# Kernel tuning notes

Measured on AMD Instinct MI355X. Metric: run time of the kernel, lower is better.

## Reference

```python
import jax, jax.numpy as jnp
import numpy as np

DIM = 384
RED = 16
PAIR = 128
EPS = 1e-5


def setup_inputs() -> dict:
    key = jax.random.key(0)
    ks = jax.random.split(key, 6)
    b, m = 2, 512
    x = jax.random.normal(ks[0], (b, m, DIM), dtype=jnp.float32)
    ln_gamma = jnp.ones((DIM,), dtype=jnp.float32)
    ln_beta = jnp.zeros((DIM,), dtype=jnp.float32)
    w_red = jax.random.normal(ks[1], (DIM, RED), dtype=jnp.float32) / np.sqrt(DIM)
    b_red = jax.random.normal(ks[2], (RED,), dtype=jnp.float32) * 0.02
    w_out = jax.random.normal(ks[3], (RED * RED, PAIR), dtype=jnp.float32) / np.sqrt(RED * RED)
    b_out = jax.random.normal(ks[4], (PAIR,), dtype=jnp.float32) * 0.02
    return {"x": x, "ln_gamma": ln_gamma, "ln_beta": ln_beta,
            "w_red": w_red, "b_red": b_red, "w_out": w_out, "b_out": b_out}


def reference(x, ln_gamma, ln_beta, w_red, b_red, w_out, b_out):
    # LayerNorm over last dim (eps=1e-5, torch default)
    mu = jnp.mean(x, axis=-1, keepdims=True)
    var = jnp.mean(jnp.square(x - mu), axis=-1, keepdims=True)
    xn = (x - mu) * jax.lax.rsqrt(var + EPS) * ln_gamma + ln_beta
    # Linear dim -> 16
    xr = jnp.einsum('bmd,dr->bmr', xn, w_red) + b_red  # (b, m, 16)
    # Full pairwise outer product + projection: same math as
    # einsum('bmi,bnj->bmnij') -> reshape (i j) -> Linear(256, pair_dim),
    # fused so the (i,j) axes contract directly with w_out reshaped to (16,16,pair).
    wr = w_out.reshape(RED, RED, PAIR)
    out = jnp.einsum('bmi,bnj,ijp->bmnp', xr, xr, wr) + b_out  # (b, m, m, pair)
    return out
```

## Files before the change

kernel.cpp:

```cpp
#include <hip/hip_runtime.h>
#include <hip/hip_bf16.h>

#define DIM 384
#define RED 16
#define PAIR 128
#define B 2
#define M 512
#define EPSV 1e-5f

typedef float f32x4 __attribute__((ext_vector_type(4)));
typedef short bf16x8 __attribute__((ext_vector_type(8)));

__device__ __forceinline__ unsigned short f2bf(float f) {
  union { float f; unsigned u; } v; v.f = f;
  unsigned r = v.u + 0x7fffu + ((v.u >> 16) & 1u);
  return (unsigned short)(r >> 16);
}

__global__ __launch_bounds__(128) void opm_k1(
    const float* __restrict__ x, const float* __restrict__ g,
    const float* __restrict__ be, const float* __restrict__ w_red,
    const float* __restrict__ b_red, const float* __restrict__ w_out,
    unsigned short* __restrict__ xr_bf, unsigned short* __restrict__ T_bf) {
  const int row = blockIdx.x;
  const int tid = threadIdx.x;
  const float* xrow = x + (size_t)row * DIM;

  __shared__ float xn[DIM];
  __shared__ float xr_s[RED];
  __shared__ float rs[2][2];
  __shared__ float psum[8][RED];

  float v0 = xrow[tid];
  float v1 = xrow[tid + 128];
  float v2 = xrow[tid + 256];
  float s  = v0 + v1 + v2;
  float sq = v0 * v0 + v1 * v1 + v2 * v2;
  #pragma unroll
  for (int off = 32; off > 0; off >>= 1) {
    s  += __shfl_down(s, off);
    sq += __shfl_down(sq, off);
  }
  if ((tid & 63) == 0) { rs[0][tid >> 6] = s; rs[1][tid >> 6] = sq; }
  __syncthreads();
  const float mean = (rs[0][0] + rs[0][1]) * (1.0f / DIM);
  const float var  = (rs[1][0] + rs[1][1]) * (1.0f / DIM) - mean * mean;
  const float rstd = rsqrtf(var + EPSV);

  xn[tid]       = (v0 - mean) * rstd * g[tid]       + be[tid];
  xn[tid + 128] = (v1 - mean) * rstd * g[tid + 128] + be[tid + 128];
  xn[tid + 256] = (v2 - mean) * rstd * g[tid + 256] + be[tid + 256];
  __syncthreads();

  {
    const int r = tid & 15;
    const int part = tid >> 4;
    float ps = 0.0f;
    const int d0 = part * 48;
    #pragma unroll 8
    for (int d = d0; d < d0 + 48; ++d) ps += xn[d] * w_red[d * RED + r];
    psum[part][r] = ps;
  }
  __syncthreads();
  if (tid < RED) {
    float v = b_red[tid];
    #pragma unroll
    for (int q = 0; q < 8; ++q) v += psum[q][tid];
    xr_s[tid] = v;
    xr_bf[(size_t)row * RED + tid] = f2bf(v);
  }
  __syncthreads();

  {
    const int p = tid;
    const float* W = w_out + p;
    float acc[RED];
    #pragma unroll
    for (int i = 0; i < RED; ++i) {
      float a = 0.0f;
      #pragma unroll
      for (int j = 0; j < RED; ++j) a += xr_s[j] * W[(i * RED + j) * PAIR];
      acc[i] = a;
    }
    unsigned int w0[4], w1[4];
    #pragma unroll
    for (int k = 0; k < 4; ++k) {
      w0[k] = (unsigned)f2bf(acc[2*k])     | ((unsigned)f2bf(acc[2*k+1]) << 16);
      w1[k] = (unsigned)f2bf(acc[8+2*k])   | ((unsigned)f2bf(acc[8+2*k+1]) << 16);
    }
    unsigned int* dst = (unsigned int*)(T_bf + ((size_t)row * PAIR + p) * RED);
    #pragma unroll
    for (int k = 0; k < 4; ++k) { dst[k] = w0[k]; dst[4+k] = w1[k]; }
  }
}

__global__ __launch_bounds__(256) void opm_k2(
    const unsigned short* __restrict__ xr_bf, const unsigned short* __restrict__ T_bf,
    const float* __restrict__ b_out, float* __restrict__ out) {
  const int nb = blockIdx.x & 127;
  const int mt = (blockIdx.x >> 7) & 7;
  const int b  = blockIdx.x >> 10;
  const int wave = threadIdx.x >> 6;
  const int lane = threadIdx.x & 63;
  const int q = lane >> 4;
  const int r = lane & 15;
  const int n = nb * 4 + wave;

  bf16x8 bv[8];
  const unsigned short* Tb = T_bf + ((size_t)(b * M + n) * PAIR) * RED;
  #pragma unroll
  for (int pb = 0; pb < 8; ++pb) {
    bf16x8 v = {0, 0, 0, 0, 0, 0, 0, 0};
    if (q < 2) v = *(const bf16x8*)(Tb + (pb * 16 + r) * RED + q * 8);
    bv[pb] = v;
  }
  float bias[8];
  #pragma unroll
  for (int pb = 0; pb < 8; ++pb) bias[pb] = b_out[pb * 16 + r];

  const size_t MROW = (size_t)M * PAIR;

  #pragma unroll
  for (int ms = 0; ms < 4; ++ms) {
    const int m0 = mt * 64 + ms * 16;
    bf16x8 av = {0, 0, 0, 0, 0, 0, 0, 0};
    if (q < 2) av = *(const bf16x8*)(xr_bf + (size_t)(b * M + m0 + r) * RED + q * 8);

    float* outbase = out + ((size_t)(b * M + m0 + q * 4) * M + n) * PAIR + r;
    #pragma unroll
    for (int pb = 0; pb < 8; ++pb) {
      f32x4 acc = {bias[pb], bias[pb], bias[pb], bias[pb]};
      acc = __builtin_amdgcn_mfma_f32_16x16x32_bf16(av, bv[pb], acc, 0, 0, 0);
      float* o = outbase + pb * 16;
      o[0]        = acc[0];
      o[MROW]     = acc[1];
      o[2 * MROW] = acc[2];
      o[3 * MROW] = acc[3];
    }
  }
}

extern "C" void kernel_launch(void* const* d_in, const int* in_sizes, int n_in,
                              void* d_out, int out_size, void* d_ws, size_t ws_size,
                              hipStream_t stream) {
  const float* x       = (const float*)d_in[0];
  const float* ln_g    = (const float*)d_in[1];
  const float* ln_b    = (const float*)d_in[2];
  const float* w_red   = (const float*)d_in[3];
  const float* b_red   = (const float*)d_in[4];
  const float* w_out   = (const float*)d_in[5];
  const float* b_out   = (const float*)d_in[6];
  float* out = (float*)d_out;

  unsigned short* xr_bf = (unsigned short*)d_ws;
  unsigned short* T_bf  = xr_bf + (size_t)B * M * RED;

  opm_k1<<<B * M, 128, 0, stream>>>(x, ln_g, ln_b, w_red, b_red, w_out, xr_bf, T_bf);
  opm_k2<<<B * (M / 64) * (M / 4), 256, 0, stream>>>(xr_bf, T_bf, b_out, out);
}
```

Measured before the change: 57.32 us.

## Stage MFMA output through LDS for vectorized stores; two rows per k1 block

```diff
diff --git a/kernel.cpp b/kernel.cpp
--- a/kernel.cpp
+++ b/kernel.cpp
@@ -7,6 +7,7 @@
 #define B 2
 #define M 512
 #define EPSV 1e-5f
+#define LSTR 133
 
 typedef float f32x4 __attribute__((ext_vector_type(4)));
 typedef short bf16x8 __attribute__((ext_vector_type(8)));
@@ -22,75 +23,81 @@
     const float* __restrict__ be, const float* __restrict__ w_red,
     const float* __restrict__ b_red, const float* __restrict__ w_out,
     unsigned short* __restrict__ xr_bf, unsigned short* __restrict__ T_bf) {
-  const int row = blockIdx.x;
-  const int tid = threadIdx.x;
-  const float* xrow = x + (size_t)row * DIM;
+  const int row0 = blockIdx.x * 2;
+  const int tid  = threadIdx.x;
+  const int wave = tid >> 6;
+  const int lane = tid & 63;
 
-  __shared__ float xn[DIM];
-  __shared__ float xr_s[RED];
-  __shared__ float rs[2][2];
-  __shared__ float psum[8][RED];
+  __shared__ float xn_s[2][DIM];
+  __shared__ float xr_s[2][RED];
+  __shared__ float psum[2][4][RED];
 
-  float v0 = xrow[tid];
-  float v1 = xrow[tid + 128];
-  float v2 = xrow[tid + 256];
-  float s  = v0 + v1 + v2;
-  float sq = v0 * v0 + v1 * v1 + v2 * v2;
-  #pragma unroll
-  for (int off = 32; off > 0; off >>= 1) {
-    s  += __shfl_down(s, off);
-    sq += __shfl_down(sq, off);
+  {
+    const int row = row0 + wave;
+    const float* xrow = x + (size_t)row * DIM;
+    float v[6];
+    #pragma unroll
+    for (int k = 0; k < 6; ++k) v[k] = xrow[lane + 64 * k];
+    float s = 0.f, sq = 0.f;
+    #pragma unroll
+    for (int k = 0; k < 6; ++k) { s += v[k]; sq += v[k] * v[k]; }
+    #pragma unroll
+    for (int off = 32; off > 0; off >>= 1) {
+      s  += __shfl_xor(s, off);
+      sq += __shfl_xor(sq, off);
+    }
+    const float mean = s * (1.0f / DIM);
+    const float var  = sq * (1.0f / DIM) - mean * mean;
+    const float rstd = rsqrtf(var + EPSV);
+    #pragma unroll
+    for (int k = 0; k < 6; ++k) {
+      const int d = lane + 64 * k;
+      xn_s[wave][d] = (v[k] - mean) * rstd * g[d] + be[d];
+    }
   }
-  if ((tid & 63) == 0) { rs[0][tid >> 6] = s; rs[1][tid >> 6] = sq; }
-  __syncthreads();
-  const float mean = (rs[0][0] + rs[0][1]) * (1.0f / DIM);
-  const float var  = (rs[1][0] + rs[1][1]) * (1.0f / DIM) - mean * mean;
-  const float rstd = rsqrtf(var + EPSV);
-
-  xn[tid]       = (v0 - mean) * rstd * g[tid]       + be[tid];
-  xn[tid + 128] = (v1 - mean) * rstd * g[tid + 128] + be[tid + 128];
-  xn[tid + 256] = (v2 - mean) * rstd * g[tid + 256] + be[tid + 256];
   __syncthreads();
 
   {
-    const int r = tid & 15;
-    const int part = tid >> 4;
-    float ps = 0.0f;
-    const int d0 = part * 48;
-    #pragma unroll 8
-    for (int d = d0; d < d0 + 48; ++d) ps += xn[d] * w_red[d * RED + r];
-    psum[part][r] = ps;
+    const int rw = wave, r = lane & 15, part = lane >> 4;
+    const int d0 = part * 96;
+    float ps = 0.f;
+    #pragma unroll 4
+    for (int d = d0; d < d0 + 96; ++d) ps += xn_s[rw][d] * w_red[d * RED + r];
+    psum[rw][part][r] = ps;
   }
   __syncthreads();
-  if (tid < RED) {
-    float v = b_red[tid];
+  if (tid < 32) {
+    const int rw = tid >> 4, r = tid & 15;
+    float v = b_red[r];
     #pragma unroll
-    for (int q = 0; q < 8; ++q) v += psum[q][tid];
-    xr_s[tid] = v;
-    xr_bf[(size_t)row * RED + tid] = f2bf(v);
+    for (int qq = 0; qq < 4; ++qq) v += psum[rw][qq][r];
+    xr_s[rw][r] = v;
+    xr_bf[(size_t)(row0 + rw) * RED + r] = f2bf(v);
   }
   __syncthreads();
 
   {
     const int p = tid;
     const float* W = w_out + p;
-    float acc[RED];
+    float a0[RED], a1[RED];
     #pragma unroll
     for (int i = 0; i < RED; ++i) {
-      float a = 0.0f;
+      float s0 = 0.f, s1 = 0.f;
       #pragma unroll
-      for (int j = 0; j < RED; ++j) a += xr_s[j] * W[(i * RED + j) * PAIR];
-      acc[i] = a;
+      for (int j = 0; j < RED; ++j) {
+        const float w = W[(i * RED + j) * PAIR];
+        s0 += xr_s[0][j] * w;
+        s1 += xr_s[1][j] * w;
+      }
+      a0[i] = s0; a1[i] = s1;
     }
-    unsigned int w0[4], w1[4];
+    unsigned int* dst0 = (unsigned int*)(T_bf + ((size_t)row0 * PAIR + p) * RED);
+    unsigned int* dst1 = (unsigned int*)(T_bf + ((size_t)(row0 + 1) * PAIR + p) * RED);
     #pragma unroll
-    for (int k = 0; k < 4; ++k) {
-      w0[k] = (unsigned)f2bf(acc[2*k])     | ((unsigned)f2bf(acc[2*k+1]) << 16);
-      w1[k] = (unsigned)f2bf(acc[8+2*k])   | ((unsigned)f2bf(acc[8+2*k+1]) << 16);
+    for (int k = 0; k < 8; ++k) {
+      dst0[k] = (unsigned)f2bf(a0[2*k]) | ((unsigned)f2bf(a0[2*k+1]) << 16);
+      dst1[k] = (unsigned)f2bf(a1[2*k]) | ((unsigned)f2bf(a1[2*k+1]) << 16);
     }
-    unsigned int* dst = (unsigned int*)(T_bf + ((size_t)row * PAIR + p) * RED);
-    #pragma unroll
-    for (int k = 0; k < 4; ++k) { dst[k] = w0[k]; dst[4+k] = w1[k]; }
   }
 }
 
@@ -100,11 +107,14 @@
   const int nb = blockIdx.x & 127;
   const int mt = (blockIdx.x >> 7) & 7;
   const int b  = blockIdx.x >> 10;
-  const int wave = threadIdx.x >> 6;
-  const int lane = threadIdx.x & 63;
+  const int tid  = threadIdx.x;
+  const int wave = tid >> 6;
+  const int lane = tid & 63;
   const int q = lane >> 4;
   const int r = lane & 15;
   const int n = nb * 4 + wave;
+
+  __shared__ float lds[64 * LSTR];
 
   bf16x8 bv[8];
   const unsigned short* Tb = T_bf + ((size_t)(b * M + n) * PAIR) * RED;
@@ -118,7 +128,10 @@
   #pragma unroll
   for (int pb = 0; pb < 8; ++pb) bias[pb] = b_out[pb * 16 + r];
 
-  const size_t MROW = (size_t)M * PAIR;
+  const int inner  = tid & 127;
+  const int n_loc  = inner >> 5;
+  const int p4     = (inner & 31) * 4;
+  const int mlb    = tid >> 7;
 
   #pragma unroll
   for (int ms = 0; ms < 4; ++ms) {
@@ -126,17 +139,26 @@
     bf16x8 av = {0, 0, 0, 0, 0, 0, 0, 0};
     if (q < 2) av = *(const bf16x8*)(xr_bf + (size_t)(b * M + m0 + r) * RED + q * 8);
 
-    float* outbase = out + ((size_t)(b * M + m0 + q * 4) * M + n) * PAIR + r;
     #pragma unroll
     for (int pb = 0; pb < 8; ++pb) {
       f32x4 acc = {bias[pb], bias[pb], bias[pb], bias[pb]};
       acc = __builtin_amdgcn_mfma_f32_16x16x32_bf16(av, bv[pb], acc, 0, 0, 0);
-      float* o = outbase + pb * 16;
-      o[0]        = acc[0];
-      o[MROW]     = acc[1];
-      o[2 * MROW] = acc[2];
-      o[3 * MROW] = acc[3];
+      float* dst = &lds[(wave * 16 + q * 4) * LSTR + pb * 16 + r];
+      dst[0]        = acc[0];
+      dst[LSTR]     = acc[1];
+      dst[2 * LSTR] = acc[2];
+      dst[3 * LSTR] = acc[3];
     }
+    __syncthreads();
+
+    float* ob = out + ((size_t)(b * M + m0 + mlb) * M + (nb * 4 + n_loc)) * PAIR + p4;
+    #pragma unroll
+    for (int ps = 0; ps < 8; ++ps) {
+      const int m_loc = mlb + ps * 2;
+      const f32x4 v = *(const f32x4*)&lds[(n_loc * 16 + m_loc) * LSTR + p4];
+      *(f32x4*)(ob + (size_t)ps * 2 * M * PAIR) = v;
+    }
+    __syncthreads();
   }
 }
 
@@ -155,6 +177,6 @@
   unsigned short* xr_bf = (unsigned short*)d_ws;
   unsigned short* T_bf  = xr_bf + (size_t)B * M * RED;
 
-  opm_k1<<<B * M, 128, 0, stream>>>(x, ln_g, ln_b, w_red, b_red, w_out, xr_bf, T_bf);
+  opm_k1<<<B * M / 2, 128, 0, stream>>>(x, ln_g, ln_b, w_red, b_red, w_out, xr_bf, T_bf);
   opm_k2<<<B * (M / 64) * (M / 4), 256, 0, stream>>>(xr_bf, T_bf, b_out, out);
 }
```

Measured after the change: 61.85 us. 1.08x slower.
